# Performance work log

Hardware: AMD Instinct MI355X
Metric: run time of the kernel (lower is better)

Reference implementation:

```python
import jax, jax.numpy as jnp
import numpy as np

N = 12000      # total nodes
T = 6000       # tail (query) nodes
H = 4000       # head (key/value) nodes
D = 256        # att_hidd_dim
NUM_HEADS = 8
HEAD_DIM = D // NUM_HEADS
EDGE_VOCAB = 64


def setup_inputs() -> dict:
    key = jax.random.key(0)
    ks = jax.random.split(key, 16)
    inp = {
        "query": jax.random.normal(ks[0], (N, D), jnp.float32),
        "key": jax.random.normal(ks[1], (N, D), jnp.float32),
        "value": jax.random.normal(ks[2], (N, D), jnp.float32),
        "adj_matrix": jax.random.randint(ks[3], (T, H), 0, 2, jnp.int32),
        "c_indices": jax.random.randint(ks[4], (T, H), 0, EDGE_VOCAB, jnp.int32),
        "ground_ind_tail": jnp.arange(T, dtype=jnp.int32),
        "ground_ind_head": jnp.arange(H, dtype=jnp.int32) + T,  # disjoint bipartite sets
        "Wq": 0.02 * jax.random.normal(ks[5], (D, D), jnp.float32),
        "bq": jnp.zeros((D,), jnp.float32),
        "Wk": 0.02 * jax.random.normal(ks[6], (D, D), jnp.float32),
        "bk": jnp.zeros((D,), jnp.float32),
        "Wv": 0.02 * jax.random.normal(ks[7], (D, D), jnp.float32),
        "bv": jnp.zeros((D,), jnp.float32),
        "Wo": 0.02 * jax.random.normal(ks[8], (D, D), jnp.float32),
        "bo": jnp.zeros((D,), jnp.float32),
        "edge_emb": 0.02 * jax.random.normal(ks[9], (EDGE_VOCAB, NUM_HEADS), jnp.float32),
    }
    return inp


def reference(query, key, value, adj_matrix, c_indices, ground_ind_tail,
              ground_ind_head, Wq, bq, Wk, bk, Wv, bv, Wo, bo, edge_emb):
    scaling = HEAD_DIM ** -0.5
    # gather + project; [heads, T, hd] / [heads, H, hd]
    q_tail = ((query[ground_ind_tail] @ Wq.T + bq) * scaling).reshape(T, NUM_HEADS, HEAD_DIM).swapaxes(0, 1)
    k_head = (key[ground_ind_head] @ Wk.T + bk).reshape(H, NUM_HEADS, HEAD_DIM).swapaxes(0, 1)
    v_head = (value[ground_ind_head] @ Wv.T + bv).reshape(H, NUM_HEADS, HEAD_DIM).swapaxes(0, 1)

    tail_mask = jnp.where(adj_matrix == 0, -1e9, 0.0)[None]              # [1, T, H]
    edge_bias = edge_emb[c_indices].transpose(2, 0, 1)                    # [heads, T, H]

    scores = jnp.einsum('htd,hsd->hts', q_tail, k_head) + tail_mask + edge_bias
    attn = jax.nn.softmax(scores, axis=-1)
    out_tail = jnp.einsum('hts,hsd->htd', attn, v_head)                   # [heads, T, hd]

    attn_all = jnp.zeros((NUM_HEADS, N, HEAD_DIM), query.dtype)
    attn_all = attn_all.at[:, ground_ind_tail].set(out_tail)
    attn_all = attn_all.at[:, ground_ind_head].set(
        query[ground_ind_head].reshape(H, NUM_HEADS, HEAD_DIM).swapaxes(0, 1))
    attn_all = attn_all.swapaxes(0, 1).reshape(N, D)                      # [N, D]
    return attn_all @ Wo.T + bo
```

## Files before the change

kernel.cpp:

```cpp
#include <hip/hip_runtime.h>
#include <hip/hip_bf16.h>

#define T_N 6000
#define H_N 4000
#define N_N 12000
#define DIM 256
#define NHEAD 8
#define HDIM 32
#define SCALING 0.17677669529663687f
#define NTT 375
#define NST 125

typedef __attribute__((ext_vector_type(8))) short bf16x8;
typedef __attribute__((ext_vector_type(4))) float f32x4;

union BF8U { bf16x8 v; unsigned int w[4]; __hip_bfloat16 h[8]; };

static __device__ __forceinline__ unsigned int cvt_pk_bf16(float a, float b) {
  unsigned int r;
  asm("v_cvt_pk_bf16_f32 %0, %1, %2" : "=v"(r) : "v"(a), "v"(b));
  return r;
}

__global__ __launch_bounds__(256) void pack_pc(
    const int* __restrict__ adj, const int* __restrict__ cind,
    unsigned int* __restrict__ pc)
{
  const int i = blockIdx.x * 256 + threadIdx.x;
  if (i >= NTT * NST * 128) return;
  const int tl = i & 15;
  const int gi = (i >> 4) & 7;
  const int rem = i >> 7;
  const int st = rem % NST;
  const int tt = rem / NST;
  const int t = tt * 16 + tl;
  const int s0 = st * 32 + gi * 4;
  const int4 c4 = *reinterpret_cast<const int4*>(cind + (size_t)t * H_N + s0);
  const int4 a4 = *reinterpret_cast<const int4*>(adj + (size_t)t * H_N + s0);
  unsigned int w = 0;
  w |= (unsigned)((c4.x & 63) | (a4.x ? 64 : 0));
  w |= (unsigned)((c4.y & 63) | (a4.y ? 64 : 0)) << 8;
  w |= (unsigned)((c4.z & 63) | (a4.z ? 64 : 0)) << 16;
  w |= (unsigned)((c4.w & 63) | (a4.w ? 64 : 0)) << 24;
  pc[i] = w;
}

template <int OM>
__global__ __launch_bounds__(256) void proj_mfma(
    const float* __restrict__ X, const int* __restrict__ idx,
    const float* __restrict__ W, const float* __restrict__ b,
    __hip_bfloat16* __restrict__ outf, int rows, float scale)
{
  __shared__ __align__(16) char As[64 * 512];
  __shared__ __align__(16) char Bs[32 * 512];

  const int tid = threadIdx.x;
  const int w = tid >> 6;
  const int lane = tid & 63;
  const int q = lane >> 4;
  const int t = lane & 15;
  const int n0 = blockIdx.x * 32;
  const int m0 = blockIdx.y * 64;

  for (int i = tid; i < 2048; i += 256) {
    const int row = i >> 5, c16 = i & 31;
    BF8U u;
    u.w[0] = 0; u.w[1] = 0; u.w[2] = 0; u.w[3] = 0;
    const int gr = m0 + row;
    if (gr < rows) {
      const int src = idx ? idx[gr] : gr;
      const float* sp = X + (size_t)src * DIM + c16 * 8;
      const float4 x0 = *reinterpret_cast<const float4*>(sp);
      const float4 x1 = *reinterpret_cast<const float4*>(sp + 4);
      u.w[0] = cvt_pk_bf16(x0.x, x0.y);
      u.w[1] = cvt_pk_bf16(x0.z, x0.w);
      u.w[2] = cvt_pk_bf16(x1.x, x1.y);
      u.w[3] = cvt_pk_bf16(x1.z, x1.w);
    }
    *reinterpret_cast<bf16x8*>(As + ((row * 512 + c16 * 16) ^ ((row & 7) << 4))) = u.v;
  }
  for (int i = tid; i < 1024; i += 256) {
    const int row = i >> 5, c16 = i & 31;
    const float* sp = W + (size_t)(n0 + row) * DIM + c16 * 8;
    const float4 x0 = *reinterpret_cast<const float4*>(sp);
    const float4 x1 = *reinterpret_cast<const float4*>(sp + 4);
    BF8U u;
    u.w[0] = cvt_pk_bf16(x0.x, x0.y);
    u.w[1] = cvt_pk_bf16(x0.z, x0.w);
    u.w[2] = cvt_pk_bf16(x1.x, x1.y);
    u.w[3] = cvt_pk_bf16(x1.z, x1.w);
    *reinterpret_cast<bf16x8*>(Bs + ((row * 512 + c16 * 16) ^ ((row & 7) << 4))) = u.v;
  }
  __syncthreads();

  f32x4 acc0 = {0.f, 0.f, 0.f, 0.f};
  f32x4 acc1 = {0.f, 0.f, 0.f, 0.f};
#pragma unroll
  for (int kk = 0; kk < 8; kk++) {
    const int arow = w * 16 + t;
    const bf16x8 af = *reinterpret_cast<const bf16x8*>(
        As + ((arow * 512 + (kk * 32 + q * 8) * 2) ^ ((arow & 7) << 4)));
    const bf16x8 bf0 = *reinterpret_cast<const bf16x8*>(
        Bs + ((t * 512 + (kk * 32 + q * 8) * 2) ^ ((t & 7) << 4)));
    const bf16x8 bf1 = *reinterpret_cast<const bf16x8*>(
        Bs + (((16 + t) * 512 + (kk * 32 + q * 8) * 2) ^ (((16 + t) & 7) << 4)));
    acc0 = __builtin_amdgcn_mfma_f32_16x16x32_bf16(af, bf0, acc0, 0, 0, 0);
    acc1 = __builtin_amdgcn_mfma_f32_16x16x32_bf16(af, bf1, acc1, 0, 0, 0);
  }

#pragma unroll
  for (int r = 0; r < 4; r++) {
    const int grow = m0 + w * 16 + q * 4 + r;
    if (grow >= rows) continue;
    const float a0 = acc0[r], a1 = acc1[r];
    const int jj[2] = {n0 + t, n0 + 16 + t};
    const float vv[2] = {(a0 + b[jj[0]]) * scale, (a1 + b[jj[1]]) * scale};
#pragma unroll
    for (int f = 0; f < 2; f++) {
      const int j = jj[f];
      const __hip_bfloat16 hv = __float2bfloat16(vv[f]);
      const int h = j >> 5;
      size_t idxo;
      if (OM == 1) {
        idxo = (((size_t)h * NTT + (grow >> 4)) * 64 + ((j & 31) >> 3) * 16 +
                (grow & 15)) * 8 + (j & 7);
      } else if (OM == 2) {
        idxo = (((size_t)h * 250 + (grow >> 4)) * 64 + ((j & 31) >> 3) * 16 +
                (grow & 15)) * 8 + (j & 7);
      } else {
        const int dh = (j & 31) >> 4, dl = j & 15;
        const int sl = grow & 31;
        const int qv = (sl & 15) >> 2;
        const int ev = (sl & 3) | (((sl >> 4) & 1) << 2);
        idxo = ((((size_t)h * 2 + dh) * NST + (grow >> 5)) * 64 +
                qv * 16 + dl) * 8 + ev;
      }
      outf[idxo] = hv;
    }
  }
}

template <bool PACKED>
__global__ __launch_bounds__(256, 5) void attn_mfma(
    const __hip_bfloat16* __restrict__ Qf, const __hip_bfloat16* __restrict__ Kf,
    const __hip_bfloat16* __restrict__ Vf, const unsigned int* __restrict__ pc,
    const int* __restrict__ adj, const int* __restrict__ cind,
    const float* __restrict__ edge_emb, const int* __restrict__ tail_idx,
    __hip_bfloat16* __restrict__ Ab)
{
  __shared__ float mg[2][64][12];

  const int tid = threadIdx.x;
  const int w = tid >> 6;
  const int lane = tid & 63;
  const int q = lane >> 4;
  const int t = lane & 15;
  const int hl = w & 1;
  const int cs = w >> 1;
  const int h = blockIdx.y * 2 + hl;
  const int tt = blockIdx.x;
  const int hbase = h * HDIM;

  const float eval = edge_emb[lane * NHEAD + h];

  const bf16x8 qf = *reinterpret_cast<const bf16x8*>(
      Qf + (((size_t)h * NTT + tt) * 64 + lane) * 8);

  const int stBeg = cs ? 63 : 0;
  const int stEnd = cs ? NST : 63;

  const unsigned int* pcp = pc + (size_t)(tt * NST + stBeg) * 128 + q * 16 + t;
  const __hip_bfloat16* kp = Kf + (((size_t)h * 250 + stBeg * 2) * 64 + lane) * 8;
  const __hip_bfloat16* vp = Vf + (((size_t)h * 2 * NST + stBeg) * 64 + lane) * 8;
  const size_t VD = (size_t)NST * 64 * 8;
  const int* crow = cind + (size_t)(tt * 16 + t) * H_N;
  const int* arow = adj + (size_t)(tt * 16 + t) * H_N;

  f32x4 oacc0 = {0.f, 0.f, 0.f, 0.f};
  f32x4 oacc1 = {0.f, 0.f, 0.f, 0.f};
  float Lacc = 0.f;

  unsigned int npc0 = 0, npc1 = 0;
  int4 ncl, nch, nal, nah;
  bf16x8 nk0, nk1, nv0, nv1;
  if (PACKED) {
    npc0 = pcp[0];
    npc1 = pcp[64];
  } else {
    const int sb = stBeg * 32 + q * 4;
    ncl = *reinterpret_cast<const int4*>(crow + sb);
    nch = *reinterpret_cast<const int4*>(crow + sb + 16);
    nal = *reinterpret_cast<const int4*>(arow + sb);
    nah = *reinterpret_cast<const int4*>(arow + sb + 16);
  }
  nk0 = *reinterpret_cast<const bf16x8*>(kp);
  nk1 = *reinterpret_cast<const bf16x8*>(kp + 512);
  nv0 = *reinterpret_cast<const bf16x8*>(vp);
  nv1 = *reinterpret_cast<const bf16x8*>(vp + VD);

  for (int st = stBeg; st < stEnd; ++st) {
    const unsigned int cpc0 = npc0, cpc1 = npc1;
    const int4 ccl = ncl, cch = nch, cal = nal, cah = nah;
    const bf16x8 kf0 = nk0, kf1 = nk1, vf0 = nv0, vf1 = nv1;

    const f32x4 z = {0.f, 0.f, 0.f, 0.f};
    const f32x4 s_lo = __builtin_amdgcn_mfma_f32_16x16x32_bf16(kf0, qf, z, 0, 0, 0);
    const f32x4 s_hi = __builtin_amdgcn_mfma_f32_16x16x32_bf16(kf1, qf, z, 0, 0, 0);

    if (st + 1 < stEnd) {
      pcp += 128; kp += 1024; vp += 512;
      if (PACKED) {
        npc0 = pcp[0];
        npc1 = pcp[64];
      } else {
        const int sb = (st + 1) * 32 + q * 4;
        ncl = *reinterpret_cast<const int4*>(crow + sb);
        nch = *reinterpret_cast<const int4*>(crow + sb + 16);
        nal = *reinterpret_cast<const int4*>(arow + sb);
        nah = *reinterpret_cast<const int4*>(arow + sb + 16);
      }
      nk0 = *reinterpret_cast<const bf16x8*>(kp);
      nk1 = *reinterpret_cast<const bf16x8*>(kp + 512);
      nv0 = *reinterpret_cast<const bf16x8*>(vp);
      nv1 = *reinterpret_cast<const bf16x8*>(vp + VD);
    }

    float p[8];
    if (PACKED) {
#pragma unroll
      for (int r = 0; r < 4; r++) {
        const unsigned b0 = (cpc0 >> (r * 8)) & 0xffu;
        const unsigned b1 = (cpc1 >> (r * 8)) & 0xffu;
        const float e0 = __shfl(eval, (int)(b0 & 63u), 64);
        const float e1 = __shfl(eval, (int)(b1 & 63u), 64);
        p[r] = s_lo[r] + ((b0 & 64u) ? e0 : -1e9f);
        p[r + 4] = s_hi[r] + ((b1 & 64u) ? e1 : -1e9f);
      }
    } else {
      const int cc[8] = {ccl.x, ccl.y, ccl.z, ccl.w, cch.x, cch.y, cch.z, cch.w};
      const int aa[8] = {cal.x, cal.y, cal.z, cal.w, cah.x, cah.y, cah.z, cah.w};
      const float sv[8] = {s_lo[0], s_lo[1], s_lo[2], s_lo[3],
                           s_hi[0], s_hi[1], s_hi[2], s_hi[3]};
#pragma unroll
      for (int r = 0; r < 8; r++) {
        const float e = __shfl(eval, cc[r] & 63, 64);
        p[r] = sv[r] + (aa[r] ? e : -1e9f);
      }
    }
#pragma unroll
    for (int r = 0; r < 8; r++) {
      p[r] = __expf(p[r]);
      Lacc += p[r];
    }

    BF8U pu;
    pu.w[0] = cvt_pk_bf16(p[0], p[1]);
    pu.w[1] = cvt_pk_bf16(p[2], p[3]);
    pu.w[2] = cvt_pk_bf16(p[4], p[5]);
    pu.w[3] = cvt_pk_bf16(p[6], p[7]);

    oacc0 = __builtin_amdgcn_mfma_f32_16x16x32_bf16(vf0, pu.v, oacc0, 0, 0, 0);
    oacc1 = __builtin_amdgcn_mfma_f32_16x16x32_bf16(vf1, pu.v, oacc1, 0, 0, 0);
  }

  Lacc += __shfl_xor(Lacc, 16, 64);
  Lacc += __shfl_xor(Lacc, 32, 64);

  if (cs) {
#pragma unroll
    for (int r = 0; r < 4; r++) {
      mg[hl][lane][r] = oacc0[r];
      mg[hl][lane][4 + r] = oacc1[r];
    }
    mg[hl][lane][8] = Lacc;
  }
  __syncthreads();
  if (!cs) {
    const float L = Lacc + mg[hl][lane][8];
    const float inv = 1.f / L;
    float o[8];
#pragma unroll
    for (int r = 0; r < 4; r++) {
      o[r] = (oacc0[r] + mg[hl][lane][r]) * inv;
      o[4 + r] = (oacc1[r] + mg[hl][lane][4 + r]) * inv;
    }
    const int row = tail_idx[tt * 16 + t];
    __hip_bfloat16* dst = Ab + (size_t)row * DIM + hbase + q * 4;
    uint2 w0, w1;
    w0.x = cvt_pk_bf16(o[0], o[1]); w0.y = cvt_pk_bf16(o[2], o[3]);
    w1.x = cvt_pk_bf16(o[4], o[5]); w1.y = cvt_pk_bf16(o[6], o[7]);
    *reinterpret_cast<uint2*>(dst) = w0;
    *reinterpret_cast<uint2*>(dst + 16) = w1;
  }
}

__global__ __launch_bounds__(64) void copy_head_rows(
    const float* __restrict__ query, const int* __restrict__ head_idx,
    __hip_bfloat16* __restrict__ Ab)
{
  const int row = head_idx[blockIdx.x];
  const int lane = threadIdx.x;
  const float4 v = *reinterpret_cast<const float4*>(
      query + (size_t)row * DIM + lane * 4);
  uint2 o;
  o.x = cvt_pk_bf16(v.x, v.y);
  o.y = cvt_pk_bf16(v.z, v.w);
  *reinterpret_cast<uint2*>(Ab + (size_t)row * DIM + lane * 4) = o;
}

__global__ __launch_bounds__(256) void oproj_mfma(
    const __hip_bfloat16* __restrict__ Ab, const float* __restrict__ Wo,
    const float* __restrict__ bo, float* __restrict__ out)
{
  __shared__ __align__(16) char As[64 * 512];
  __shared__ __align__(16) char Bs[32 * 512];

  const int tid = threadIdx.x;
  const int w = tid >> 6;
  const int lane = tid & 63;
  const int bl = lane & 15;
  const int q = lane >> 4;
  const int n0 = blockIdx.x * 32;
  const int m0 = blockIdx.y * 64;

  for (int i = tid; i < 2048; i += 256) {
    const int row = i >> 5, c16 = i & 31;
    bf16x8 v = {0, 0, 0, 0, 0, 0, 0, 0};
    const int gr = m0 + row;
    if (gr < N_N)
      v = *reinterpret_cast<const bf16x8*>(Ab + (size_t)gr * DIM + c16 * 8);
    *reinterpret_cast<bf16x8*>(As + ((row * 512 + c16 * 16) ^ ((row & 7) << 4))) = v;
  }
  for (int i = tid; i < 1024; i += 256) {
    const int row = i >> 5, c16 = i & 31;
    const float* src = Wo + (size_t)(n0 + row) * DIM + c16 * 8;
    const float4 x0 = *reinterpret_cast<const float4*>(src);
    const float4 x1 = *reinterpret_cast<const float4*>(src + 4);
    BF8U u;
    u.w[0] = cvt_pk_bf16(x0.x, x0.y);
    u.w[1] = cvt_pk_bf16(x0.z, x0.w);
    u.w[2] = cvt_pk_bf16(x1.x, x1.y);
    u.w[3] = cvt_pk_bf16(x1.z, x1.w);
    *reinterpret_cast<bf16x8*>(Bs + ((row * 512 + c16 * 16) ^ ((row & 7) << 4))) = u.v;
  }
  __syncthreads();

  f32x4 acc0 = {0.f, 0.f, 0.f, 0.f};
  f32x4 acc1 = {0.f, 0.f, 0.f, 0.f};
#pragma unroll
  for (int kk = 0; kk < 8; kk++) {
    const int arow = w * 16 + bl;
    const bf16x8 af = *reinterpret_cast<const bf16x8*>(
        As + ((arow * 512 + (kk * 32 + q * 8) * 2) ^ ((arow & 7) << 4)));
    const bf16x8 bf0 = *reinterpret_cast<const bf16x8*>(
        Bs + ((bl * 512 + (kk * 32 + q * 8) * 2) ^ ((bl & 7) << 4)));
    const int brow = 16 + bl;
    const bf16x8 bf1 = *reinterpret_cast<const bf16x8*>(
        Bs + ((brow * 512 + (kk * 32 + q * 8) * 2) ^ ((brow & 7) << 4)));
    acc0 = __builtin_amdgcn_mfma_f32_16x16x32_bf16(af, bf0, acc0, 0, 0, 0);
    acc1 = __builtin_amdgcn_mfma_f32_16x16x32_bf16(af, bf1, acc1, 0, 0, 0);
  }

#pragma unroll
  for (int r = 0; r < 4; r++) {
    const int grow = m0 + w * 16 + q * 4 + r;
    if (grow < N_N) {
      const int j0 = n0 + bl;
      const int j1 = n0 + 16 + bl;
      out[(size_t)grow * DIM + j0] = acc0[r] + bo[j0];
      out[(size_t)grow * DIM + j1] = acc1[r] + bo[j1];
    }
  }
}

extern "C" void kernel_launch(void* const* d_in, const int* in_sizes, int n_in,
                              void* d_out, int out_size, void* d_ws, size_t ws_size,
                              hipStream_t stream)
{
  const float* query    = (const float*)d_in[0];
  const float* key      = (const float*)d_in[1];
  const float* value    = (const float*)d_in[2];
  const int*   adj      = (const int*)d_in[3];
  const int*   cind     = (const int*)d_in[4];
  const int*   tail_idx = (const int*)d_in[5];
  const int*   head_idx = (const int*)d_in[6];
  const float* Wq = (const float*)d_in[7];
  const float* bq = (const float*)d_in[8];
  const float* Wk = (const float*)d_in[9];
  const float* bk = (const float*)d_in[10];
  const float* Wv = (const float*)d_in[11];
  const float* bv = (const float*)d_in[12];
  const float* Wo = (const float*)d_in[13];
  const float* bo = (const float*)d_in[14];
  const float* edge_emb = (const float*)d_in[15];

  float* out = (float*)d_out;
  char*  ws  = (char*)d_ws;

  __hip_bfloat16* Ab = (__hip_bfloat16*)ws;
  __hip_bfloat16* Qf = (__hip_bfloat16*)(ws + 6144000);
  __hip_bfloat16* Kf = (__hip_bfloat16*)(ws + 9216000);
  __hip_bfloat16* Vf = (__hip_bfloat16*)(ws + 11264000);
  unsigned int*   pc = (unsigned int*)(ws + 13312000);
  const bool packed = ws_size >= (size_t)37312000;

  hipMemsetAsync(Ab, 0, (size_t)N_N * DIM * sizeof(__hip_bfloat16), stream);

  if (packed)
    pack_pc<<<dim3((NTT * NST * 128 + 255) / 256), dim3(256), 0, stream>>>(
        adj, cind, pc);

  const dim3 blk(256);
  proj_mfma<1><<<dim3(8, (T_N + 63) / 64), blk, 0, stream>>>(
      query, tail_idx, Wq, bq, Qf, T_N, SCALING);
  proj_mfma<2><<<dim3(8, (H_N + 63) / 64), blk, 0, stream>>>(
      key, head_idx, Wk, bk, Kf, H_N, 1.f);
  proj_mfma<3><<<dim3(8, (H_N + 63) / 64), blk, 0, stream>>>(
      value, head_idx, Wv, bv, Vf, H_N, 1.f);

  if (packed)
    attn_mfma<true><<<dim3(NTT, 4), blk, 0, stream>>>(
        Qf, Kf, Vf, pc, adj, cind, edge_emb, tail_idx, Ab);
  else
    attn_mfma<false><<<dim3(NTT, 4), blk, 0, stream>>>(
        Qf, Kf, Vf, pc, adj, cind, edge_emb, tail_idx, Ab);

  copy_head_rows<<<dim3(H_N), dim3(64), 0, stream>>>(query, head_idx, Ab);

  oproj_mfma<<<dim3(8, (N_N + 63) / 64), blk, 0, stream>>>(
      Ab, Wo, bo, out);
}
```

Measured before the change: 172.2 us.

## Fuse pre-attention kernels, split key range over four waves, use exp2 with bpermute

Merges the Q/K/V projections, the head-row copy and the adjacency/edge-index packing into one launch that dispatches on block index, which cuts launch count and lets independent work overlap. The attention kernel now gives one head per block and splits the key tiles across four waves, merging partial sums through shared memory. Occupancy hint is raised to 8. Softmax uses exp2 with log2e folded into the Q scaling and the edge table, and the edge-bias lookup uses ds_bpermute on a repacked byte layout. The non-packed fallback path is removed, so the workspace must always be large enough, and the larger reduction adds shared-memory traffic.

Result: faster. 168.2 us (-2.3%).

```diff
diff --git a/kernel.cpp b/kernel.cpp
--- a/kernel.cpp
+++ b/kernel.cpp
@@ -8,6 +8,7 @@
 #define NHEAD 8
 #define HDIM 32
 #define SCALING 0.17677669529663687f
+#define LOG2E 1.4426950408889634f
 #define NTT 375
 #define NST 125
 
@@ -22,45 +23,19 @@
   return r;
 }
 
-__global__ __launch_bounds__(256) void pack_pc(
-    const int* __restrict__ adj, const int* __restrict__ cind,
-    unsigned int* __restrict__ pc)
+static __device__ __forceinline__ void proj_body(
+    int role, const float* __restrict__ X, const int* __restrict__ idx,
+    const float* __restrict__ W, const float* __restrict__ bvec,
+    __hip_bfloat16* __restrict__ outf, int rows, float scale, int bx,
+    char* As, char* Bs)
 {
-  const int i = blockIdx.x * 256 + threadIdx.x;
-  if (i >= NTT * NST * 128) return;
-  const int tl = i & 15;
-  const int gi = (i >> 4) & 7;
-  const int rem = i >> 7;
-  const int st = rem % NST;
-  const int tt = rem / NST;
-  const int t = tt * 16 + tl;
-  const int s0 = st * 32 + gi * 4;
-  const int4 c4 = *reinterpret_cast<const int4*>(cind + (size_t)t * H_N + s0);
-  const int4 a4 = *reinterpret_cast<const int4*>(adj + (size_t)t * H_N + s0);
-  unsigned int w = 0;
-  w |= (unsigned)((c4.x & 63) | (a4.x ? 64 : 0));
-  w |= (unsigned)((c4.y & 63) | (a4.y ? 64 : 0)) << 8;
-  w |= (unsigned)((c4.z & 63) | (a4.z ? 64 : 0)) << 16;
-  w |= (unsigned)((c4.w & 63) | (a4.w ? 64 : 0)) << 24;
-  pc[i] = w;
-}
-
-template <int OM>
-__global__ __launch_bounds__(256) void proj_mfma(
-    const float* __restrict__ X, const int* __restrict__ idx,
-    const float* __restrict__ W, const float* __restrict__ b,
-    __hip_bfloat16* __restrict__ outf, int rows, float scale)
-{
-  __shared__ __align__(16) char As[64 * 512];
-  __shared__ __align__(16) char Bs[32 * 512];
-
   const int tid = threadIdx.x;
   const int w = tid >> 6;
   const int lane = tid & 63;
   const int q = lane >> 4;
   const int t = lane & 15;
-  const int n0 = blockIdx.x * 32;
-  const int m0 = blockIdx.y * 64;
+  const int n0 = (bx & 7) * 32;
+  const int m0 = (bx >> 3) * 64;
 
   for (int i = tid; i < 2048; i += 256) {
     const int row = i >> 5, c16 = i & 31;
@@ -114,17 +89,17 @@
     if (grow >= rows) continue;
     const float a0 = acc0[r], a1 = acc1[r];
     const int jj[2] = {n0 + t, n0 + 16 + t};
-    const float vv[2] = {(a0 + b[jj[0]]) * scale, (a1 + b[jj[1]]) * scale};
+    const float vv[2] = {(a0 + bvec[jj[0]]) * scale, (a1 + bvec[jj[1]]) * scale};
 #pragma unroll
     for (int f = 0; f < 2; f++) {
       const int j = jj[f];
       const __hip_bfloat16 hv = __float2bfloat16(vv[f]);
       const int h = j >> 5;
       size_t idxo;
-      if (OM == 1) {
+      if (role == 1) {
         idxo = (((size_t)h * NTT + (grow >> 4)) * 64 + ((j & 31) >> 3) * 16 +
                 (grow & 15)) * 8 + (j & 7);
-      } else if (OM == 2) {
+      } else if (role == 2) {
         idxo = (((size_t)h * 250 + (grow >> 4)) * 64 + ((j & 31) >> 3) * 16 +
                 (grow & 15)) * 8 + (j & 7);
       } else {
@@ -140,67 +115,108 @@
   }
 }
 
-template <bool PACKED>
-__global__ __launch_bounds__(256, 5) void attn_mfma(
+#define NBQ 752
+#define NBK 504
+#define NBV 504
+#define NBC 1000
+#define NBP 23438
+
+__global__ __launch_bounds__(256) void fused_pre(
+    const float* __restrict__ query, const float* __restrict__ key,
+    const float* __restrict__ value, const int* __restrict__ adj,
+    const int* __restrict__ cind, const int* __restrict__ tail_idx,
+    const int* __restrict__ head_idx,
+    const float* __restrict__ Wq, const float* __restrict__ bq,
+    const float* __restrict__ Wk, const float* __restrict__ bk,
+    const float* __restrict__ Wv, const float* __restrict__ bv,
+    __hip_bfloat16* __restrict__ Qf, __hip_bfloat16* __restrict__ Kf,
+    __hip_bfloat16* __restrict__ Vf, unsigned int* __restrict__ pc,
+    __hip_bfloat16* __restrict__ Ab)
+{
+  __shared__ __align__(16) char As[64 * 512];
+  __shared__ __align__(16) char Bs[32 * 512];
+
+  const int bx = blockIdx.x;
+  if (bx < NBQ) {
+    proj_body(1, query, tail_idx, Wq, bq, Qf, T_N, SCALING * LOG2E, bx, As, Bs);
+  } else if (bx < NBQ + NBK) {
+    proj_body(2, key, head_idx, Wk, bk, Kf, H_N, 1.f, bx - NBQ, As, Bs);
+  } else if (bx < NBQ + NBK + NBV) {
+    proj_body(3, value, head_idx, Wv, bv, Vf, H_N, 1.f, bx - NBQ - NBK, As, Bs);
+  } else if (bx < NBQ + NBK + NBV + NBC) {
+    const int b = bx - NBQ - NBK - NBV;
+    const int rr = b * 4 + (threadIdx.x >> 6);
+    const int lane = threadIdx.x & 63;
+    const int row = head_idx[rr];
+    const float4 v = *reinterpret_cast<const float4*>(
+        query + (size_t)row * DIM + lane * 4);
+    uint2 o;
+    o.x = cvt_pk_bf16(v.x, v.y);
+    o.y = cvt_pk_bf16(v.z, v.w);
+    *reinterpret_cast<uint2*>(Ab + (size_t)row * DIM + lane * 4) = o;
+  } else {
+    const int i = (bx - NBQ - NBK - NBV - NBC) * 256 + threadIdx.x;
+    if (i >= NTT * NST * 128) return;
+    const int tl = i & 15;
+    const int gi = (i >> 4) & 7;
+    const int rem = i >> 7;
+    const int st = rem % NST;
+    const int tt = rem / NST;
+    const int t = tt * 16 + tl;
+    const int s0 = st * 32 + gi * 4;
+    const int4 c4 = *reinterpret_cast<const int4*>(cind + (size_t)t * H_N + s0);
+    const int4 a4 = *reinterpret_cast<const int4*>(adj + (size_t)t * H_N + s0);
+    unsigned int w = 0;
+    w |= (unsigned)(((c4.x & 63) << 2) | (a4.x ? 1 : 0));
+    w |= (unsigned)(((c4.y & 63) << 2) | (a4.y ? 1 : 0)) << 8;
+    w |= (unsigned)(((c4.z & 63) << 2) | (a4.z ? 1 : 0)) << 16;
+    w |= (unsigned)(((c4.w & 63) << 2) | (a4.w ? 1 : 0)) << 24;
+    pc[i] = w;
+  }
+}
+
+__global__ __launch_bounds__(256, 8) void attn_mfma(
     const __hip_bfloat16* __restrict__ Qf, const __hip_bfloat16* __restrict__ Kf,
     const __hip_bfloat16* __restrict__ Vf, const unsigned int* __restrict__ pc,
-    const int* __restrict__ adj, const int* __restrict__ cind,
     const float* __restrict__ edge_emb, const int* __restrict__ tail_idx,
     __hip_bfloat16* __restrict__ Ab)
 {
-  __shared__ float mg[2][64][12];
+  __shared__ float mg[3][64][10];
 
   const int tid = threadIdx.x;
-  const int w = tid >> 6;
+  const int cs = tid >> 6;
   const int lane = tid & 63;
   const int q = lane >> 4;
   const int t = lane & 15;
-  const int hl = w & 1;
-  const int cs = w >> 1;
-  const int h = blockIdx.y * 2 + hl;
+  const int h = blockIdx.y;
   const int tt = blockIdx.x;
   const int hbase = h * HDIM;
 
-  const float eval = edge_emb[lane * NHEAD + h];
+  const int etab = __float_as_int(edge_emb[lane * NHEAD + h] * LOG2E);
 
   const bf16x8 qf = *reinterpret_cast<const bf16x8*>(
       Qf + (((size_t)h * NTT + tt) * 64 + lane) * 8);
 
-  const int stBeg = cs ? 63 : 0;
-  const int stEnd = cs ? NST : 63;
+  const int stBeg = (cs * NST) >> 2;
+  const int stEnd = ((cs + 1) * NST) >> 2;
 
   const unsigned int* pcp = pc + (size_t)(tt * NST + stBeg) * 128 + q * 16 + t;
   const __hip_bfloat16* kp = Kf + (((size_t)h * 250 + stBeg * 2) * 64 + lane) * 8;
   const __hip_bfloat16* vp = Vf + (((size_t)h * 2 * NST + stBeg) * 64 + lane) * 8;
   const size_t VD = (size_t)NST * 64 * 8;
-  const int* crow = cind + (size_t)(tt * 16 + t) * H_N;
-  const int* arow = adj + (size_t)(tt * 16 + t) * H_N;
 
   f32x4 oacc0 = {0.f, 0.f, 0.f, 0.f};
   f32x4 oacc1 = {0.f, 0.f, 0.f, 0.f};
   float Lacc = 0.f;
 
-  unsigned int npc0 = 0, npc1 = 0;
-  int4 ncl, nch, nal, nah;
-  bf16x8 nk0, nk1, nv0, nv1;
-  if (PACKED) {
-    npc0 = pcp[0];
-    npc1 = pcp[64];
-  } else {
-    const int sb = stBeg * 32 + q * 4;
-    ncl = *reinterpret_cast<const int4*>(crow + sb);
-    nch = *reinterpret_cast<const int4*>(crow + sb + 16);
-    nal = *reinterpret_cast<const int4*>(arow + sb);
-    nah = *reinterpret_cast<const int4*>(arow + sb + 16);
-  }
-  nk0 = *reinterpret_cast<const bf16x8*>(kp);
-  nk1 = *reinterpret_cast<const bf16x8*>(kp + 512);
-  nv0 = *reinterpret_cast<const bf16x8*>(vp);
-  nv1 = *reinterpret_cast<const bf16x8*>(vp + VD);
+  unsigned int npc0 = pcp[0], npc1 = pcp[64];
+  bf16x8 nk0 = *reinterpret_cast<const bf16x8*>(kp);
+  bf16x8 nk1 = *reinterpret_cast<const bf16x8*>(kp + 512);
+  bf16x8 nv0 = *reinterpret_cast<const bf16x8*>(vp);
+  bf16x8 nv1 = *reinterpret_cast<const bf16x8*>(vp + VD);
 
   for (int st = stBeg; st < stEnd; ++st) {
     const unsigned int cpc0 = npc0, cpc1 = npc1;
-    const int4 ccl = ncl, cch = nch, cal = nal, cah = nah;
     const bf16x8 kf0 = nk0, kf1 = nk1, vf0 = nv0, vf1 = nv1;
 
     const f32x4 z = {0.f, 0.f, 0.f, 0.f};
@@ -209,16 +225,8 @@
 
     if (st + 1 < stEnd) {
       pcp += 128; kp += 1024; vp += 512;
-      if (PACKED) {
-        npc0 = pcp[0];
-        npc1 = pcp[64];
-      } else {
-        const int sb = (st + 1) * 32 + q * 4;
-        ncl = *reinterpret_cast<const int4*>(crow + sb);
-        nch = *reinterpret_cast<const int4*>(crow + sb + 16);
-        nal = *reinterpret_cast<const int4*>(arow + sb);
-        nah = *reinterpret_cast<const int4*>(arow + sb + 16);
-      }
+      npc0 = pcp[0];
+      npc1 = pcp[64];
       nk0 = *reinterpret_cast<const bf16x8*>(kp);
       nk1 = *reinterpret_cast<const bf16x8*>(kp + 512);
       nv0 = *reinterpret_cast<const bf16x8*>(vp);
@@ -226,32 +234,19 @@
     }
 
     float p[8];
-    if (PACKED) {
-#pragma unroll
-      for (int r = 0; r < 4; r++) {
-        const unsigned b0 = (cpc0 >> (r * 8)) & 0xffu;
-        const unsigned b1 = (cpc1 >> (r * 8)) & 0xffu;
-        const float e0 = __shfl(eval, (int)(b0 & 63u), 64);
-        const float e1 = __shfl(eval, (int)(b1 & 63u), 64);
-        p[r] = s_lo[r] + ((b0 & 64u) ? e0 : -1e9f);
-        p[r + 4] = s_hi[r] + ((b1 & 64u) ? e1 : -1e9f);
-      }
-    } else {
-      const int cc[8] = {ccl.x, ccl.y, ccl.z, ccl.w, cch.x, cch.y, cch.z, cch.w};
-      const int aa[8] = {cal.x, cal.y, cal.z, cal.w, cah.x, cah.y, cah.z, cah.w};
-      const float sv[8] = {s_lo[0], s_lo[1], s_lo[2], s_lo[3],
-                           s_hi[0], s_hi[1], s_hi[2], s_hi[3]};
-#pragma unroll
-      for (int r = 0; r < 8; r++) {
-        const float e = __shfl(eval, cc[r] & 63, 64);
-        p[r] = sv[r] + (aa[r] ? e : -1e9f);
-      }
-    }
-#pragma unroll
-    for (int r = 0; r < 8; r++) {
-      p[r] = __expf(p[r]);
-      Lacc += p[r];
-    }
+#pragma unroll
+    for (int r = 0; r < 4; r++) {
+      const unsigned b0 = (cpc0 >> (r * 8)) & 0xffu;
+      const unsigned b1 = (cpc1 >> (r * 8)) & 0xffu;
+      const int e0 = __builtin_amdgcn_ds_bpermute((int)(b0 & 0xfcu), etab);
+      const int e1 = __builtin_amdgcn_ds_bpermute((int)(b1 & 0xfcu), etab);
+      const float bb0 = (b0 & 1u) ? __int_as_float(e0) : -1e9f;
+      const float bb1 = (b1 & 1u) ? __int_as_float(e1) : -1e9f;
+      p[r] = __builtin_amdgcn_exp2f(s_lo[r] + bb0);
+      p[r + 4] = __builtin_amdgcn_exp2f(s_hi[r] + bb1);
+    }
+#pragma unroll
+    for (int r = 0; r < 8; r++) Lacc += p[r];
 
     BF8U pu;
     pu.w[0] = cvt_pk_bf16(p[0], p[1]);
@@ -269,43 +264,34 @@
   if (cs) {
 #pragma unroll
     for (int r = 0; r < 4; r++) {
-      mg[hl][lane][r] = oacc0[r];
-      mg[hl][lane][4 + r] = oacc1[r];
-    }
-    mg[hl][lane][8] = Lacc;
+      mg[cs - 1][lane][r] = oacc0[r];
+      mg[cs - 1][lane][4 + r] = oacc1[r];
+    }
+    mg[cs - 1][lane][8] = Lacc;
   }
   __syncthreads();
   if (!cs) {
-    const float L = Lacc + mg[hl][lane][8];
+    float L = Lacc;
+    float o[8];
+#pragma unroll
+    for (int r = 0; r < 8; r++) o[r] = (r < 4) ? oacc0[r] : oacc1[r - 4];
+#pragma unroll
+    for (int c = 0; c < 3; c++) {
+      L += mg[c][lane][8];
+#pragma unroll
+      for (int r = 0; r < 8; r++) o[r] += mg[c][lane][r];
+    }
     const float inv = 1.f / L;
-    float o[8];
-#pragma unroll
-    for (int r = 0; r < 4; r++) {
-      o[r] = (oacc0[r] + mg[hl][lane][r]) * inv;
-      o[4 + r] = (oacc1[r] + mg[hl][lane][4 + r]) * inv;
-    }
     const int row = tail_idx[tt * 16 + t];
     __hip_bfloat16* dst = Ab + (size_t)row * DIM + hbase + q * 4;
     uint2 w0, w1;
-    w0.x = cvt_pk_bf16(o[0], o[1]); w0.y = cvt_pk_bf16(o[2], o[3]);
-    w1.x = cvt_pk_bf16(o[4], o[5]); w1.y = cvt_pk_bf16(o[6], o[7]);
+    w0.x = cvt_pk_bf16(o[0] * inv, o[1] * inv);
+    w0.y = cvt_pk_bf16(o[2] * inv, o[3] * inv);
+    w1.x = cvt_pk_bf16(o[4] * inv, o[5] * inv);
+    w1.y = cvt_pk_bf16(o[6] * inv, o[7] * inv);
     *reinterpret_cast<uint2*>(dst) = w0;
     *reinterpret_cast<uint2*>(dst + 16) = w1;
   }
-}
-
-__global__ __launch_bounds__(64) void copy_head_rows(
-    const float* __restrict__ query, const int* __restrict__ head_idx,
-    __hip_bfloat16* __restrict__ Ab)
-{
-  const int row = head_idx[blockIdx.x];
-  const int lane = threadIdx.x;
-  const float4 v = *reinterpret_cast<const float4*>(
-      query + (size_t)row * DIM + lane * 4);
-  uint2 o;
-  o.x = cvt_pk_bf16(v.x, v.y);
-  o.y = cvt_pk_bf16(v.z, v.w);
-  *reinterpret_cast<uint2*>(Ab + (size_t)row * DIM + lane * 4) = o;
 }
 
 __global__ __launch_bounds__(256) void oproj_mfma(
@@ -402,31 +388,16 @@
   __hip_bfloat16* Kf = (__hip_bfloat16*)(ws + 9216000);
   __hip_bfloat16* Vf = (__hip_bfloat16*)(ws + 11264000);
   unsigned int*   pc = (unsigned int*)(ws + 13312000);
-  const bool packed = ws_size >= (size_t)37312000;
 
   hipMemsetAsync(Ab, 0, (size_t)N_N * DIM * sizeof(__hip_bfloat16), stream);
 
-  if (packed)
-    pack_pc<<<dim3((NTT * NST * 128 + 255) / 256), dim3(256), 0, stream>>>(
-        adj, cind, pc);
-
-  const dim3 blk(256);
-  proj_mfma<1><<<dim3(8, (T_N + 63) / 64), blk, 0, stream>>>(
-      query, tail_idx, Wq, bq, Qf, T_N, SCALING);
-  proj_mfma<2><<<dim3(8, (H_N + 63) / 64), blk, 0, stream>>>(
-      key, head_idx, Wk, bk, Kf, H_N, 1.f);
-  proj_mfma<3><<<dim3(8, (H_N + 63) / 64), blk, 0, stream>>>(
-      value, head_idx, Wv, bv, Vf, H_N, 1.f);
-
-  if (packed)
-    attn_mfma<true><<<dim3(NTT, 4), blk, 0, stream>>>(
-        Qf, Kf, Vf, pc, adj, cind, edge_emb, tail_idx, Ab);
-  else
-    attn_mfma<false><<<dim3(NTT, 4), blk, 0, stream>>>(
-        Qf, Kf, Vf, pc, adj, cind, edge_emb, tail_idx, Ab);
-
-  copy_head_rows<<<dim3(H_N), dim3(64), 0, stream>>>(query, head_idx, Ab);
-
-  oproj_mfma<<<dim3(8, (N_N + 63) / 64), blk, 0, stream>>>(
+  fused_pre<<<dim3(NBQ + NBK + NBV + NBC + NBP), dim3(256), 0, stream>>>(
+      query, key, value, adj, cind, tail_idx, head_idx,
+      Wq, bq, Wk, bk, Wv, bv, Qf, Kf, Vf, pc, Ab);
+
+  attn_mfma<<<dim3(NTT, NHEAD), dim3(256), 0, stream>>>(
+      Qf, Kf, Vf, pc, edge_emb, tail_idx, Ab);
+
+  oproj_mfma<<<dim3(8, (N_N + 63) / 64), dim3(256), 0, stream>>>(
       Ab, Wo, bo, out);
 }
```
